# Optimization experiments

Hardware: AMD Instinct MI355X
Metric: run time of the kernel (lower is better)

Reference implementation:

```python
import jax, jax.numpy as jnp
import numpy as np

B = 512       # number of graphs
MAX_N = 128   # pad length (>= max(num_atoms))
D = 256       # emb_dim


def setup_inputs() -> dict:
    key = jax.random.key(0)
    ks = jax.random.split(key, 20)
    num_atoms_np = np.full(B, 80, dtype=np.int64)
    num_atoms_np[: B // 2] = 112
    num_atoms_np[B // 2 :] = 48
    total = int(num_atoms_np.sum())  # 40960, static
    scale = 1.0 / np.sqrt(D)

    def lin_w(k):
        return jax.random.normal(k, (D, D), jnp.float32) * scale

    inp = {
        'rep_2d': jax.random.normal(ks[0], (total, D), jnp.float32),
        'rep_3d': jax.random.normal(ks[1], (total, D), jnp.float32),
        'num_atoms': jnp.asarray(num_atoms_np),
        # mha_2d_3d (queries from 2d, keys/values from 3d)
        'wq23': lin_w(ks[2]), 'bq23': jnp.zeros((D,), jnp.float32),
        'wk23': lin_w(ks[3]), 'bk23': jnp.zeros((D,), jnp.float32),
        'wv23': lin_w(ks[4]), 'bv23': jnp.zeros((D,), jnp.float32),
        # mha_3d_2d (queries from 3d, keys/values from 2d)
        'wq32': lin_w(ks[5]), 'bq32': jnp.zeros((D,), jnp.float32),
        'wk32': lin_w(ks[6]), 'bk32': jnp.zeros((D,), jnp.float32),
        'wv32': lin_w(ks[7]), 'bv32': jnp.zeros((D,), jnp.float32),
        # per-branch Linear (normalizer=Identity) + GELU
        'wm23': lin_w(ks[8]), 'bm23': jnp.zeros((D,), jnp.float32),
        'wm32': lin_w(ks[9]), 'bm32': jnp.zeros((D,), jnp.float32),
    }
    return inp


def _variadic_to_padded(flat, num_atoms):
    # flat: [total, D] -> padded [B, MAX_N, D], mask [B, MAX_N] (True = valid)
    cum = jnp.cumsum(num_atoms)
    offsets = cum - num_atoms
    pos = jnp.arange(MAX_N)
    mask = pos[None, :] < num_atoms[:, None]
    idx = jnp.where(mask, offsets[:, None] + pos[None, :], 0)
    padded = flat[idx] * mask[..., None].astype(flat.dtype)
    return padded, mask


def _padded_to_variadic(padded, num_atoms, total):
    # padded: [B, MAX_N, D] -> flat [total, D]
    cum = jnp.cumsum(num_atoms)
    t = jnp.arange(total)
    b = jnp.searchsorted(cum, t, side='right')
    i = t - (cum - num_atoms)[b]
    return padded[b, i]


def _cross_attn(q_in, kv_in, mask, wq, bq, wk, bk, wv, bv):
    # single-head scaled dot-product cross-attention, key-side padding mask
    q = q_in @ wq.T + bq
    k = kv_in @ wk.T + bk
    v = kv_in @ wv.T + bv
    s = jnp.einsum('bqd,bkd->bqk', q, k) / jnp.sqrt(jnp.asarray(D, q.dtype))
    s = jnp.where(mask[:, None, :], s, jnp.asarray(-1e9, s.dtype))
    a = jax.nn.softmax(s, axis=-1)
    return jnp.einsum('bqk,bkd->bqd', a, v)


def reference(rep_2d, rep_3d, num_atoms,
              wq23, bq23, wk23, bk23, wv23, bv23,
              wq32, bq32, wk32, bk32, wv32, bv32,
              wm23, bm23, wm32, bm32):
    total = rep_2d.shape[0]
    p2d, mask = _variadic_to_padded(rep_2d, num_atoms)
    p3d, _ = _variadic_to_padded(rep_3d, num_atoms)
    x2d = _cross_attn(p2d, p3d, mask, wq23, bq23, wk23, bk23, wv23, bv23)
    x3d = _cross_attn(p3d, p2d, mask, wq32, bq32, wk32, bk32, wv32, bv32)
    x2d = _padded_to_variadic(x2d, num_atoms, total)
    x3d = _padded_to_variadic(x3d, num_atoms, total)
    out2d = jax.nn.gelu(x2d @ wm23.T + bm23, approximate=False)
    out3d = jax.nn.gelu(x3d @ wm32.T + bm32, approximate=False)
    return (out2d, out3d)
```

## Files before the change

kernel.cpp:

```cpp
#include <hip/hip_runtime.h>
#include <hip/hip_bf16.h>
#include <cstdint>


typedef short s16x8 __attribute__((ext_vector_type(8)));
typedef float f32x4 __attribute__((ext_vector_type(4)));

__device__ __forceinline__ s16x8 cvt8(const float* p) {
  float4 a0 = *(const float4*)p, a1 = *(const float4*)(p + 4);
  union { s16x8 v; __bf16 e[8]; } u;
  u.e[0] = (__bf16)a0.x; u.e[1] = (__bf16)a0.y; u.e[2] = (__bf16)a0.z; u.e[3] = (__bf16)a0.w;
  u.e[4] = (__bf16)a1.x; u.e[5] = (__bf16)a1.y; u.e[6] = (__bf16)a1.z; u.e[7] = (__bf16)a1.w;
  return u.v;
}
__device__ __forceinline__ float fast_gelu(float x) {
  float ax = fabsf(x);
  float t = 1.0f / (1.0f + 0.3275911f * (ax * 0.70710678f));
  float y = t * (0.254829592f + t * (-0.284496736f + t * (1.421413741f +
            t * (-1.453152027f + t * 1.061405429f))));
  float er = 1.0f - y * __expf(-0.5f * ax * ax);
  er = (x < 0.f) ? -er : er;
  return 0.5f * x * (1.0f + er);
}

__global__ void sentinel_kernel(float* out, float v) {
  if (threadIdx.x == 0 && blockIdx.x == 0) out[0] = v;
}

__global__ __launch_bounds__(512) void scan_kernel(
    const int* __restrict__ na, int* __restrict__ offs,
    int B, int total, float* out)
{
  __shared__ int s32[512];
  __shared__ int s64[512];
  const int t = threadIdx.x;
  int v32 = 0, v64 = 0;
  if (t < B) {
    v32 = na[t];
    v64 = (int)((const long long*)na)[t];
  }
  s32[t] = v32; s64[t] = v64;
  __syncthreads();
  for (int o = 1; o < 512; o <<= 1) {
    int a = (t >= o) ? s32[t - o] : 0;
    int b = (t >= o) ? s64[t - o] : 0;
    __syncthreads();
    s32[t] += a; s64[t] += b;
    __syncthreads();
  }
  int tot32 = s32[B - 1], tot64 = s64[B - 1];
  bool ok32 = (tot32 == total), ok64 = (tot64 == total);
  if (t < B) offs[t] = ok32 ? (s32[t] - v32) : ok64 ? (s64[t] - v64) : 0;
  if (t == 0) {
    offs[B] = ok32 ? tot32 : ok64 ? tot64 : 0;
    if (!ok32 && !ok64) out[0] = 31337.0f;
  }
}

__global__ __launch_bounds__(256) void cvt_kernel(
    const float* __restrict__ in, __bf16* __restrict__ out) {
  int i = (blockIdx.x * 256 + threadIdx.x) * 4;
  float4 f = *(const float4*)(in + i);
  out[i + 0] = (__bf16)f.x; out[i + 1] = (__bf16)f.y;
  out[i + 2] = (__bf16)f.z; out[i + 3] = (__bf16)f.w;
}

__global__ __launch_bounds__(256) void gemm_kernel(
    const float* __restrict__ A, const float* __restrict__ Bw,
    const float* __restrict__ bias, __bf16* __restrict__ C, int N)
{
  __shared__ __bf16 At[128 * 32];
  __shared__ __bf16 Bt[128 * 32];
  const int t = threadIdx.x;
  const int lane = t & 63, w = t >> 6;
  const int wr = w >> 1, wc = w & 1;
  const int l15 = lane & 15, l4 = lane >> 4;
  const int by = blockIdx.x, bx = blockIdx.y;

  f32x4 acc[4][4];
  for (int m = 0; m < 4; ++m)
    for (int nn = 0; nn < 4; ++nn) acc[m][nn] = (f32x4){0.f, 0.f, 0.f, 0.f};

  for (int kk = 0; kk < 256; kk += 32) {
    for (int j = 0; j < 2; ++j) {
      int c = t + j * 256;
      int row = c >> 2, off0 = (c & 3) * 8;
      *(s16x8*)(&At[row * 32 + off0]) = cvt8(A + (size_t)(by * 128 + row) * 256 + kk + off0);
      *(s16x8*)(&Bt[row * 32 + off0]) = cvt8(Bw + (size_t)(bx * 128 + row) * 256 + kk + off0);
    }
    __syncthreads();
    s16x8 af[4], bfr[4];
    for (int m = 0; m < 4; ++m)
      af[m] = *(const s16x8*)(&At[(wr * 64 + m * 16 + l15) * 32 + l4 * 8]);
    for (int nn = 0; nn < 4; ++nn)
      bfr[nn] = *(const s16x8*)(&Bt[(wc * 64 + nn * 16 + l15) * 32 + l4 * 8]);
    for (int m = 0; m < 4; ++m)
      for (int nn = 0; nn < 4; ++nn)
        acc[m][nn] = __builtin_amdgcn_mfma_f32_16x16x32_bf16(af[m], bfr[nn], acc[m][nn], 0, 0, 0);
    __syncthreads();
  }

  for (int m = 0; m < 4; ++m) {
    int row0 = by * 128 + wr * 64 + m * 16 + l4 * 4;
    for (int nn = 0; nn < 4; ++nn) {
      int col = bx * 128 + wc * 64 + nn * 16 + l15;
      float bc = bias[col];
      for (int r = 0; r < 4; ++r) {
        int row = row0 + r;
        C[(size_t)row * N + col] = (__bf16)(acc[m][nn][r] + bc);
      }
    }
  }
}

#define CTP 136
__global__ __launch_bounds__(256) void vgemm_kernel(
    const float* __restrict__ A, const float* __restrict__ Bw,
    const float* __restrict__ bias, __bf16* __restrict__ Vt, int total)
{
  __shared__ __bf16 At[128 * 32];
  __shared__ __bf16 Bt[128 * 32];
  __shared__ __bf16 Ct[128 * CTP];
  const int t = threadIdx.x;
  const int lane = t & 63, w = t >> 6;
  const int wr = w >> 1, wc = w & 1;
  const int l15 = lane & 15, l4 = lane >> 4;
  const int by = blockIdx.x, bx = blockIdx.y;

  f32x4 acc[4][4];
  for (int m = 0; m < 4; ++m)
    for (int nn = 0; nn < 4; ++nn) acc[m][nn] = (f32x4){0.f, 0.f, 0.f, 0.f};

  for (int kk = 0; kk < 256; kk += 32) {
    for (int j = 0; j < 2; ++j) {
      int c = t + j * 256;
      int row = c >> 2, off0 = (c & 3) * 8;
      *(s16x8*)(&At[row * 32 + off0]) = cvt8(A + (size_t)(by * 128 + row) * 256 + kk + off0);
      *(s16x8*)(&Bt[row * 32 + off0]) = cvt8(Bw + (size_t)(bx * 128 + row) * 256 + kk + off0);
    }
    __syncthreads();
    s16x8 af[4], bfr[4];
    for (int m = 0; m < 4; ++m)
      af[m] = *(const s16x8*)(&At[(wr * 64 + m * 16 + l15) * 32 + l4 * 8]);
    for (int nn = 0; nn < 4; ++nn)
      bfr[nn] = *(const s16x8*)(&Bt[(wc * 64 + nn * 16 + l15) * 32 + l4 * 8]);
    for (int m = 0; m < 4; ++m)
      for (int nn = 0; nn < 4; ++nn)
        acc[m][nn] = __builtin_amdgcn_mfma_f32_16x16x32_bf16(af[m], bfr[nn], acc[m][nn], 0, 0, 0);
    __syncthreads();
  }

  for (int m = 0; m < 4; ++m) {
    int rl0 = wr * 64 + m * 16 + l4 * 4;
    for (int nn = 0; nn < 4; ++nn) {
      int cl = wc * 64 + nn * 16 + l15;
      for (int r = 0; r < 4; ++r) {
        int rl = rl0 + r;
        Ct[rl * CTP + cl] = (__bf16)(acc[m][nn][r] + bias[by * 128 + rl]);
      }
    }
  }
  __syncthreads();

  for (int i = 0; i < 8; ++i) {
    int c = t + i * 256;
    int row = c >> 4, seg = c & 15;
    *(uint4*)(Vt + (size_t)(by * 128 + row) * total + bx * 128 + seg * 8) =
        *(const uint4*)(&Ct[row * CTP + seg * 8]);
  }
}

struct Attn2Args {
  const __bf16* Q[2]; const __bf16* K[2]; const __bf16* V[2];
  unsigned long long X[2];
};
#define KSTR 264
#define PSTR 136
__global__ __launch_bounds__(512, 2) void attn2_kernel(
    Attn2Args args, const int* __restrict__ offs, int total)
{
  __shared__ __bf16 smem[128 * KSTR];
  __bf16 (*Klds)[KSTR] = (__bf16(*)[KSTR])smem;
  __bf16 (*Plds)[PSTR] = (__bf16(*)[PSTR])smem;
  __bf16 (*XT)[KSTR]   = (__bf16(*)[KSTR])smem;

  const int br = blockIdx.y;
  const __bf16* Q  = args.Q[br];
  const __bf16* Km = args.K[br];
  const __bf16* Vt = args.V[br];
  __bf16* X = (__bf16*)args.X[br];

  const int g = blockIdx.x;
  const int off = offs[g];
  const int n = offs[g + 1] - off;
  const int t = threadIdx.x, lane = t & 63, w = t >> 6;
  const int l15 = lane & 15, l4 = lane >> 4;
  const bool qact = (w * 16) < n;

  uint4 kst[8];
  #pragma unroll
  for (int j = 0; j < 8; ++j) {
    int row = j * 16 + (t >> 5);
    kst[j] = *(const uint4*)((const char*)(Km + (size_t)(off + row) * 256) + (t & 31) * 16);
  }
  s16x8 qf[8];
  if (qact) {
    int qr = w * 16 + l15; if (qr >= n) qr = n - 1;
    const __bf16* qp = Q + (size_t)(off + qr) * 256 + l4 * 8;
    #pragma unroll
    for (int kk = 0; kk < 8; ++kk) qf[kk] = *(const s16x8*)(qp + kk * 32);
  }
  #pragma unroll
  for (int j = 0; j < 8; ++j) {
    int row = j * 16 + (t >> 5);
    *(uint4*)((char*)&Klds[row][0] + (t & 31) * 16) = kst[j];
  }
  __syncthreads();

  f32x4 sacc[8];
  #pragma unroll
  for (int i = 0; i < 8; ++i) sacc[i] = (f32x4){0.f, 0.f, 0.f, 0.f};
  if (qact) {
    #pragma unroll
    for (int kt = 0; kt < 8; ++kt) {
      if (kt * 16 < n) {
        const __bf16* kp = &Klds[kt * 16 + l15][l4 * 8];
        #pragma unroll
        for (int kk = 0; kk < 8; ++kk) {
          s16x8 kf = *(const s16x8*)(kp + kk * 32);
          sacc[kt] = __builtin_amdgcn_mfma_f32_16x16x32_bf16(qf[kk], kf, sacc[kt], 0, 0, 0);
        }
      }
    }
  }
  __syncthreads();

  if (qact) {
    #pragma unroll
    for (int r = 0; r < 4; ++r) {
      float sv[8];
      float m = -1e30f;
      #pragma unroll
      for (int kt = 0; kt < 8; ++kt) {
        int key = kt * 16 + l15;
        float v = (key < n) ? sacc[kt][r] * 0.0625f : -1e30f;
        sv[kt] = v; m = fmaxf(m, v);
      }
      for (int o = 1; o < 16; o <<= 1) m = fmaxf(m, __shfl_xor(m, o));
      float p[8], sum = 0.f;
      #pragma unroll
      for (int kt = 0; kt < 8; ++kt) { p[kt] = __expf(sv[kt] - m); sum += p[kt]; }
      for (int o = 1; o < 16; o <<= 1) sum += __shfl_xor(sum, o);
      float inv = 1.f / sum;
      int q = w * 16 + l4 * 4 + r;
      #pragma unroll
      for (int kt = 0; kt < 8; ++kt)
        Plds[q][kt * 16 + l15] = (__bf16)(p[kt] * inv);
    }
  }
  __syncthreads();

  const int dbase = w * 32;
  f32x4 xacc[2][8];
  #pragma unroll
  for (int dt = 0; dt < 2; ++dt)
    #pragma unroll
    for (int qm = 0; qm < 8; ++qm) xacc[dt][qm] = (f32x4){0.f, 0.f, 0.f, 0.f};

  #pragma unroll
  for (int dt = 0; dt < 2; ++dt) {
    int d = dbase + dt * 16 + l15;
    s16x8 vf[4];
    #pragma unroll
    for (int ks = 0; ks < 4; ++ks) {
      int kc = off + ks * 32 + l4 * 8;
      if (kc > total - 8) kc = total - 8;
      vf[ks] = *(const s16x8*)(Vt + (size_t)d * total + kc);
    }
    #pragma unroll
    for (int qm = 0; qm < 8; ++qm) {
      #pragma unroll
      for (int ks = 0; ks < 4; ++ks) {
        if (ks * 32 < n) {
          s16x8 pa = *(const s16x8*)(&Plds[qm * 16 + l15][ks * 32 + l4 * 8]);
          xacc[dt][qm] = __builtin_amdgcn_mfma_f32_16x16x32_bf16(pa, vf[ks], xacc[dt][qm], 0, 0, 0);
        }
      }
    }
  }
  __syncthreads();

  #pragma unroll
  for (int dt = 0; dt < 2; ++dt)
    #pragma unroll
    for (int qm = 0; qm < 8; ++qm)
      #pragma unroll
      for (int r = 0; r < 4; ++r)
        XT[qm * 16 + l4 * 4 + r][dbase + dt * 16 + l15] = (__bf16)xacc[dt][qm][r];
  __syncthreads();

  #pragma unroll
  for (int i = 0; i < 8; ++i) {
    int c = t + i * 512;
    int row = c >> 5, seg = c & 31;
    if (row < n)
      *(uint4*)(X + (size_t)(off + row) * 256 + seg * 8) =
          *(const uint4*)(&XT[row][seg * 8]);
  }
}

__global__ __launch_bounds__(256) void gemm_out(
    const __bf16* __restrict__ A, const __bf16* __restrict__ W,
    const float* __restrict__ bias, float* __restrict__ C)
{
  __shared__ __bf16 At[64 * 32];
  __shared__ __bf16 Bt[128 * 32];
  const int t = threadIdx.x;
  const int lane = t & 63, w = t >> 6;
  const int wr = w >> 1, wc = w & 1;
  const int l15 = lane & 15, l4 = lane >> 4;
  const int by = blockIdx.x, bx = blockIdx.y;

  f32x4 acc[2][4];
  for (int m = 0; m < 2; ++m)
    for (int nn = 0; nn < 4; ++nn) acc[m][nn] = (f32x4){0.f, 0.f, 0.f, 0.f};

  for (int kk = 0; kk < 256; kk += 32) {
    {
      int row = t >> 2, off0 = (t & 3) * 8;
      *(s16x8*)(&At[row * 32 + off0]) =
          *(const s16x8*)(A + (size_t)(by * 64 + row) * 256 + kk + off0);
    }
    for (int j = 0; j < 2; ++j) {
      int c = t + j * 256;
      int row = c >> 2, off0 = (c & 3) * 8;
      *(s16x8*)(&Bt[row * 32 + off0]) =
          *(const s16x8*)(W + (size_t)(bx * 128 + row) * 256 + kk + off0);
    }
    __syncthreads();
    s16x8 af[2], bfr[4];
    for (int m = 0; m < 2; ++m)
      af[m] = *(const s16x8*)(&At[(wr * 32 + m * 16 + l15) * 32 + l4 * 8]);
    for (int nn = 0; nn < 4; ++nn)
      bfr[nn] = *(const s16x8*)(&Bt[(wc * 64 + nn * 16 + l15) * 32 + l4 * 8]);
    for (int m = 0; m < 2; ++m)
      for (int nn = 0; nn < 4; ++nn)
        acc[m][nn] = __builtin_amdgcn_mfma_f32_16x16x32_bf16(af[m], bfr[nn], acc[m][nn], 0, 0, 0);
    __syncthreads();
  }

  for (int m = 0; m < 2; ++m) {
    int row0 = by * 64 + wr * 32 + m * 16 + l4 * 4;
    for (int nn = 0; nn < 4; ++nn) {
      int col = bx * 128 + wc * 64 + nn * 16 + l15;
      float bc = bias[col];
      for (int r = 0; r < 4; ++r) {
        int row = row0 + r;
        C[(size_t)row * 256 + col] = fast_gelu(acc[m][nn][r] + bc);
      }
    }
  }
}

extern "C" void kernel_launch(void* const* d_in, const int* in_sizes, int n_in,
                              void* d_out, int out_size, void* d_ws, size_t ws_size,
                              hipStream_t stream) {
  const float* rep2d = (const float*)d_in[0];
  const float* rep3d = (const float*)d_in[1];
  const int*   na    = (const int*)d_in[2];
  const float* wq23 = (const float*)d_in[3];  const float* bq23 = (const float*)d_in[4];
  const float* wk23 = (const float*)d_in[5];  const float* bk23 = (const float*)d_in[6];
  const float* wv23 = (const float*)d_in[7];  const float* bv23 = (const float*)d_in[8];
  const float* wq32 = (const float*)d_in[9];  const float* bq32 = (const float*)d_in[10];
  const float* wk32 = (const float*)d_in[11]; const float* bk32 = (const float*)d_in[12];
  const float* wv32 = (const float*)d_in[13]; const float* bv32 = (const float*)d_in[14];
  const float* wm23 = (const float*)d_in[15]; const float* bm23 = (const float*)d_in[16];
  const float* wm32 = (const float*)d_in[17]; const float* bm32 = (const float*)d_in[18];

  const int B = in_sizes[2];
  const int total = in_sizes[0] / 256;
  float* out = (float*)d_out;

  char* ws = (char*)d_ws;
  const size_t SZ = (size_t)total * 256 * sizeof(__bf16);
  const size_t WMB = 65536 * sizeof(__bf16);
  const size_t need6 = 8192 + 2 * WMB + 6 * SZ;
  const size_t need3 = 8192 + 2 * WMB + 3 * SZ;
  int* offs = (int*)ws;

  dim3 blk(256);
  dim3 blkA(512);
  dim3 gP(total / 128, 2);
  dim3 gV(2, total / 128);
  dim3 gO(total / 64, 2);

  if (ws_size >= need6) {
    __bf16* WM0 = (__bf16*)(ws + 8192);
    __bf16* WM1 = (__bf16*)(ws + 8192 + WMB);
    __bf16* BQ1 = (__bf16*)(ws + 8192 + 2 * WMB);
    __bf16* BK1 = (__bf16*)(ws + 8192 + 2 * WMB + SZ);
    __bf16* BV1 = (__bf16*)(ws + 8192 + 2 * WMB + 2 * SZ);
    __bf16* BQ2 = (__bf16*)(ws + 8192 + 2 * WMB + 3 * SZ);
    __bf16* BK2 = (__bf16*)(ws + 8192 + 2 * WMB + 4 * SZ);
    __bf16* BV2 = (__bf16*)(ws + 8192 + 2 * WMB + 5 * SZ);

    scan_kernel<<<1, 512, 0, stream>>>(na, offs, B, total, out);
    cvt_kernel<<<64, blk, 0, stream>>>(wm23, WM0);
    cvt_kernel<<<64, blk, 0, stream>>>(wm32, WM1);
    gemm_kernel<<<gP, blk, 0, stream>>>(rep2d, wq23, bq23, BQ1, 256);
    gemm_kernel<<<gP, blk, 0, stream>>>(rep3d, wk23, bk23, BK1, 256);
    vgemm_kernel<<<gV, blk, 0, stream>>>(wv23, rep3d, bv23, BV1, total);
    gemm_kernel<<<gP, blk, 0, stream>>>(rep3d, wq32, bq32, BQ2, 256);
    gemm_kernel<<<gP, blk, 0, stream>>>(rep2d, wk32, bk32, BK2, 256);
    vgemm_kernel<<<gV, blk, 0, stream>>>(wv32, rep2d, bv32, BV2, total);

    Attn2Args aa;
    aa.Q[0] = BQ1; aa.K[0] = BK1; aa.V[0] = BV1; aa.X[0] = (unsigned long long)BQ1;
    aa.Q[1] = BQ2; aa.K[1] = BK2; aa.V[1] = BV2; aa.X[1] = (unsigned long long)BQ2;
    attn2_kernel<<<dim3(B, 2), blkA, 0, stream>>>(aa, offs, total);

    gemm_out<<<gO, blk, 0, stream>>>(BQ1, WM0, bm23, out);
    gemm_out<<<gO, blk, 0, stream>>>(BQ2, WM1, bm32, out + (size_t)total * 256);
  } else if (ws_size >= need3) {
    __bf16* WM0 = (__bf16*)(ws + 8192);
    __bf16* WM1 = (__bf16*)(ws + 8192 + WMB);
    __bf16* BQ = (__bf16*)(ws + 8192 + 2 * WMB);
    __bf16* BK = (__bf16*)(ws + 8192 + 2 * WMB + SZ);
    __bf16* BV = (__bf16*)(ws + 8192 + 2 * WMB + 2 * SZ);

    scan_kernel<<<1, 512, 0, stream>>>(na, offs, B, total, out);
    cvt_kernel<<<64, blk, 0, stream>>>(wm23, WM0);
    cvt_kernel<<<64, blk, 0, stream>>>(wm32, WM1);
    for (int br = 0; br < 2; ++br) {
      const float* rq = br ? rep3d : rep2d;
      const float* rk = br ? rep2d : rep3d;
      const float* wq = br ? wq32 : wq23;  const float* bq = br ? bq32 : bq23;
      const float* wk = br ? wk32 : wk23;  const float* bk = br ? bk32 : bk23;
      const float* wv = br ? wv32 : wv23;  const float* bv = br ? bv32 : bv23;
      __bf16* wm = br ? WM1 : WM0;         const float* bm = br ? bm32 : bm23;
      float* o = out + (size_t)br * total * 256;

      gemm_kernel<<<gP, blk, 0, stream>>>(rq, wq, bq, BQ, 256);
      gemm_kernel<<<gP, blk, 0, stream>>>(rk, wk, bk, BK, 256);
      vgemm_kernel<<<gV, blk, 0, stream>>>(wv, rk, bv, BV, total);
      Attn2Args aa;
      aa.Q[0] = BQ; aa.K[0] = BK; aa.V[0] = BV; aa.X[0] = (unsigned long long)BQ;
      aa.Q[1] = BQ; aa.K[1] = BK; aa.V[1] = BV; aa.X[1] = (unsigned long long)BQ;
      attn2_kernel<<<dim3(B, 1), blkA, 0, stream>>>(aa, offs, total);
      gemm_out<<<gO, blk, 0, stream>>>(BQ, wm, bm, o);
    }
  } else {
    sentinel_kernel<<<1, 64, 0, stream>>>(out, 54321.0f);
  }
}
```

Before: 211.3 us.

## Halve attention LDS footprint by staging K and X in two 64-row passes

Shrinks the attention kernel's shared buffer from 128x264 to 128x136 bf16 by loading K, computing scores, and writing back X in two 64-row halves, with the second half done only when a graph has more than 64 atoms. The smaller LDS footprint is meant to let more 512-thread blocks reside per CU and skip unused work for small graphs. It costs extra barriers and sequentialises the second K half behind the first. The two weight-conversion launches are also merged into one kernel with a 2D grid.

New measurement: 214.6 us. Within noise of the previous version (+1.5%).

```diff
diff --git a/kernel.cpp b/kernel.cpp
--- a/kernel.cpp
+++ b/kernel.cpp
@@ -57,8 +57,11 @@
   }
 }
 
-__global__ __launch_bounds__(256) void cvt_kernel(
-    const float* __restrict__ in, __bf16* __restrict__ out) {
+__global__ __launch_bounds__(256) void cvt2_kernel(
+    const float* __restrict__ in0, const float* __restrict__ in1,
+    __bf16* __restrict__ out0, __bf16* __restrict__ out1) {
+  const float* in = blockIdx.y ? in1 : in0;
+  __bf16* out = blockIdx.y ? out1 : out0;
   int i = (blockIdx.x * 256 + threadIdx.x) * 4;
   float4 f = *(const float4*)(in + i);
   out[i + 0] = (__bf16)f.x; out[i + 1] = (__bf16)f.y;
@@ -174,15 +177,16 @@
   const __bf16* Q[2]; const __bf16* K[2]; const __bf16* V[2];
   unsigned long long X[2];
 };
-#define KSTR 264
-#define PSTR 136
+#define KP 264
+#define PP 136
+#define XP 272
 __global__ __launch_bounds__(512, 2) void attn2_kernel(
     Attn2Args args, const int* __restrict__ offs, int total)
 {
-  __shared__ __bf16 smem[128 * KSTR];
-  __bf16 (*Klds)[KSTR] = (__bf16(*)[KSTR])smem;
-  __bf16 (*Plds)[PSTR] = (__bf16(*)[PSTR])smem;
-  __bf16 (*XT)[KSTR]   = (__bf16(*)[KSTR])smem;
+  __shared__ __bf16 smem[128 * 136];
+  __bf16 (*Klds)[KP] = (__bf16(*)[KP])smem;
+  __bf16 (*Plds)[PP] = (__bf16(*)[PP])smem;
+  __bf16 (*XT)[XP]   = (__bf16(*)[XP])smem;
 
   const int br = blockIdx.y;
   const __bf16* Q  = args.Q[br];
@@ -196,13 +200,13 @@
   const int t = threadIdx.x, lane = t & 63, w = t >> 6;
   const int l15 = lane & 15, l4 = lane >> 4;
   const bool qact = (w * 16) < n;
-
-  uint4 kst[8];
-  #pragma unroll
-  for (int j = 0; j < 8; ++j) {
-    int row = j * 16 + (t >> 5);
-    kst[j] = *(const uint4*)((const char*)(Km + (size_t)(off + row) * 256) + (t & 31) * 16);
-  }
+  const bool big = (n > 64);
+
+  const int srow = t >> 5, scol = (t & 31) * 16;
+  uint4 kst[4];
+  #pragma unroll
+  for (int j = 0; j < 4; ++j)
+    kst[j] = *(const uint4*)((const char*)(Km + (size_t)(off + j * 16 + srow) * 256) + scol);
   s16x8 qf[8];
   if (qact) {
     int qr = w * 16 + l15; if (qr >= n) qr = n - 1;
@@ -211,9 +215,13 @@
     for (int kk = 0; kk < 8; ++kk) qf[kk] = *(const s16x8*)(qp + kk * 32);
   }
   #pragma unroll
-  for (int j = 0; j < 8; ++j) {
-    int row = j * 16 + (t >> 5);
-    *(uint4*)((char*)&Klds[row][0] + (t & 31) * 16) = kst[j];
+  for (int j = 0; j < 4; ++j)
+    *(uint4*)((char*)&Klds[j * 16 + srow][0] + scol) = kst[j];
+  uint4 kst1[4];
+  if (big) {
+    #pragma unroll
+    for (int j = 0; j < 4; ++j)
+      kst1[j] = *(const uint4*)((const char*)(Km + (size_t)(off + 64 + j * 16 + srow) * 256) + scol);
   }
   __syncthreads();
 
@@ -222,18 +230,34 @@
   for (int i = 0; i < 8; ++i) sacc[i] = (f32x4){0.f, 0.f, 0.f, 0.f};
   if (qact) {
     #pragma unroll
-    for (int kt = 0; kt < 8; ++kt) {
-      if (kt * 16 < n) {
+    for (int kt = 0; kt < 4; ++kt) {
+      const __bf16* kp = &Klds[kt * 16 + l15][l4 * 8];
+      #pragma unroll
+      for (int kk = 0; kk < 8; ++kk) {
+        s16x8 kf = *(const s16x8*)(kp + kk * 32);
+        sacc[kt] = __builtin_amdgcn_mfma_f32_16x16x32_bf16(qf[kk], kf, sacc[kt], 0, 0, 0);
+      }
+    }
+  }
+  __syncthreads();
+  if (big) {
+    #pragma unroll
+    for (int j = 0; j < 4; ++j)
+      *(uint4*)((char*)&Klds[j * 16 + srow][0] + scol) = kst1[j];
+    __syncthreads();
+    if (qact) {
+      #pragma unroll
+      for (int kt = 0; kt < 4; ++kt) {
         const __bf16* kp = &Klds[kt * 16 + l15][l4 * 8];
         #pragma unroll
         for (int kk = 0; kk < 8; ++kk) {
           s16x8 kf = *(const s16x8*)(kp + kk * 32);
-          sacc[kt] = __builtin_amdgcn_mfma_f32_16x16x32_bf16(qf[kk], kf, sacc[kt], 0, 0, 0);
+          sacc[4 + kt] = __builtin_amdgcn_mfma_f32_16x16x32_bf16(qf[kk], kf, sacc[4 + kt], 0, 0, 0);
         }
       }
     }
-  }
-  __syncthreads();
+    __syncthreads();
+  }
 
   if (qact) {
     #pragma unroll
@@ -254,8 +278,13 @@
       float inv = 1.f / sum;
       int q = w * 16 + l4 * 4 + r;
       #pragma unroll
-      for (int kt = 0; kt < 8; ++kt)
+      for (int kt = 0; kt < 4; ++kt)
         Plds[q][kt * 16 + l15] = (__bf16)(p[kt] * inv);
+      if (big) {
+        #pragma unroll
+        for (int kt = 4; kt < 8; ++kt)
+          Plds[q][kt * 16 + l15] = (__bf16)(p[kt] * inv);
+      }
     }
   }
   __syncthreads();
@@ -293,19 +322,38 @@
   #pragma unroll
   for (int dt = 0; dt < 2; ++dt)
     #pragma unroll
-    for (int qm = 0; qm < 8; ++qm)
+    for (int qm = 0; qm < 4; ++qm)
       #pragma unroll
       for (int r = 0; r < 4; ++r)
         XT[qm * 16 + l4 * 4 + r][dbase + dt * 16 + l15] = (__bf16)xacc[dt][qm][r];
   __syncthreads();
-
-  #pragma unroll
-  for (int i = 0; i < 8; ++i) {
+  #pragma unroll
+  for (int i = 0; i < 4; ++i) {
     int c = t + i * 512;
     int row = c >> 5, seg = c & 31;
     if (row < n)
       *(uint4*)(X + (size_t)(off + row) * 256 + seg * 8) =
           *(const uint4*)(&XT[row][seg * 8]);
+  }
+  if (big) {
+    __syncthreads();
+    #pragma unroll
+    for (int dt = 0; dt < 2; ++dt)
+      #pragma unroll
+      for (int qm = 4; qm < 8; ++qm)
+        #pragma unroll
+        for (int r = 0; r < 4; ++r)
+          XT[(qm - 4) * 16 + l4 * 4 + r][dbase + dt * 16 + l15] = (__bf16)xacc[dt][qm][r];
+    __syncthreads();
+    #pragma unroll
+    for (int i = 0; i < 4; ++i) {
+      int c = t + i * 512;
+      int row = c >> 5, seg = c & 31;
+      int grow = 64 + row;
+      if (grow < n)
+        *(uint4*)(X + (size_t)(off + grow) * 256 + seg * 8) =
+            *(const uint4*)(&XT[row][seg * 8]);
+    }
   }
 }
 
@@ -405,8 +453,7 @@
     __bf16* BV2 = (__bf16*)(ws + 8192 + 2 * WMB + 5 * SZ);
 
     scan_kernel<<<1, 512, 0, stream>>>(na, offs, B, total, out);
-    cvt_kernel<<<64, blk, 0, stream>>>(wm23, WM0);
-    cvt_kernel<<<64, blk, 0, stream>>>(wm32, WM1);
+    cvt2_kernel<<<dim3(64, 2), blk, 0, stream>>>(wm23, wm32, WM0, WM1);
     gemm_kernel<<<gP, blk, 0, stream>>>(rep2d, wq23, bq23, BQ1, 256);
     gemm_kernel<<<gP, blk, 0, stream>>>(rep3d, wk23, bk23, BK1, 256);
     vgemm_kernel<<<gV, blk, 0, stream>>>(wv23, rep3d, bv23, BV1, total);
@@ -429,8 +476,7 @@
     __bf16* BV = (__bf16*)(ws + 8192 + 2 * WMB + 2 * SZ);
 
     scan_kernel<<<1, 512, 0, stream>>>(na, offs, B, total, out);
-    cvt_kernel<<<64, blk, 0, stream>>>(wm23, WM0);
-    cvt_kernel<<<64, blk, 0, stream>>>(wm32, WM1);
+    cvt2_kernel<<<dim3(64, 2), blk, 0, stream>>>(wm23, wm32, WM0, WM1);
     for (int br = 0; br < 2; ++br) {
       const float* rq = br ? rep3d : rep2d;
       const float* rk = br ? rep2d : rep3d;
```
